# Kernel tuning notes

Measured on AMD Instinct MI355X. Metric: run time of the kernel, lower is better.

The kernel has to match this reference:

```python
import jax, jax.numpy as jnp
import numpy as np

N_NODES = 20000
N_EDGES = 160000
N_GRAPHS = 64
HIDDEN = 128
CTX = 2048
HEADS = 4
NUM_LAYERS = 3
NUM_BINS = 240
MAX_DIST = 30.0
GAMMA = 0.5
BN_EPS = 1e-5
OUT_DIM = 1024


def setup_inputs() -> dict:
    key = jax.random.key(0)
    ks = jax.random.split(key, 32)
    inp = {}
    inp["atom_types"] = jax.random.randint(ks[0], (N_NODES,), 0, 118)
    inp["pos"] = jax.random.normal(ks[1], (N_NODES, 3), dtype=jnp.float32) * 5.0
    inp["edge_index"] = jax.random.randint(ks[2], (2, N_EDGES), 0, N_NODES)
    inp["edge_attr"] = jax.random.uniform(ks[3], (N_EDGES, 5), dtype=jnp.float32)
    inp["batch"] = jnp.sort(jax.random.randint(ks[4], (N_NODES,), 0, N_GRAPHS))
    inp["context_vector"] = jax.random.normal(ks[5], (N_GRAPHS, CTX), dtype=jnp.float32)
    # initial node embedding Linear(118 -> 128)
    inp["emb_W"] = jax.random.normal(ks[6], (118, HIDDEN), dtype=jnp.float32) * 0.05
    inp["emb_b"] = jnp.zeros((HIDDEN,), jnp.float32)
    # RBF positional MLP: Linear(720->128) + BN + ReLU + Linear(128->2048)
    inp["rbf_lin1_W"] = jax.random.normal(ks[7], (3 * NUM_BINS, 128), dtype=jnp.float32) * 0.03
    inp["rbf_lin1_b"] = jnp.zeros((128,), jnp.float32)
    inp["rbf_bn_g"] = jnp.ones((128,), jnp.float32)
    inp["rbf_bn_b"] = jnp.zeros((128,), jnp.float32)
    inp["rbf_bn_m"] = jax.random.normal(ks[8], (128,), dtype=jnp.float32) * 0.1
    inp["rbf_bn_v"] = jax.random.uniform(ks[9], (128,), dtype=jnp.float32, minval=0.5, maxval=1.5)
    inp["rbf_lin2_W"] = jax.random.normal(ks[10], (128, CTX), dtype=jnp.float32) * 0.05
    inp["rbf_lin2_b"] = jnp.zeros((CTX,), jnp.float32)
    # per-layer GAT params (stacked over layers)
    in_dim = HIDDEN + CTX  # 2176
    inp["gat_W"] = jax.random.normal(ks[11], (NUM_LAYERS, in_dim, HEADS * HIDDEN), dtype=jnp.float32) * 0.02
    inp["att_src"] = jax.random.normal(ks[12], (NUM_LAYERS, HEADS, HIDDEN), dtype=jnp.float32) * 0.1
    inp["att_dst"] = jax.random.normal(ks[13], (NUM_LAYERS, HEADS, HIDDEN), dtype=jnp.float32) * 0.1
    inp["gat_bias"] = jnp.zeros((NUM_LAYERS, HIDDEN), jnp.float32)
    inp["bn_g"] = jnp.ones((NUM_LAYERS, HIDDEN), jnp.float32)
    inp["bn_b"] = jnp.zeros((NUM_LAYERS, HIDDEN), jnp.float32)
    inp["bn_m"] = jax.random.normal(ks[14], (NUM_LAYERS, HIDDEN), dtype=jnp.float32) * 0.1
    inp["bn_v"] = jax.random.uniform(ks[15], (NUM_LAYERS, HIDDEN), dtype=jnp.float32, minval=0.5, maxval=1.5)
    # final Linear(128 -> 1024)
    inp["out_W"] = jax.random.normal(ks[16], (HIDDEN, OUT_DIM), dtype=jnp.float32) * 0.05
    inp["out_b"] = jnp.zeros((OUT_DIM,), jnp.float32)
    return inp


def _bn_eval(x, g, b, m, v):
    return (x - m) * jax.lax.rsqrt(v + BN_EPS) * g + b


def _forward(atom_types, pos, edge_index, edge_attr, batch, context_vector,
             emb_W, emb_b, rbf_lin1_W, rbf_lin1_b, rbf_bn_g, rbf_bn_b, rbf_bn_m,
             rbf_bn_v, rbf_lin2_W, rbf_lin2_b, gat_W, att_src, att_dst, gat_bias,
             bn_g, bn_b, bn_m, bn_v, out_W, out_b):
    N = atom_types.shape[0]
    # initial node embedding (one-hot @ W == row gather, but keep faithful math)
    x = jax.nn.one_hot(atom_types, 118, dtype=jnp.float32) @ emb_W + emb_b  # [N,128]
    # RBF positional encoding: [N,3,num_bins] -> [N,720]
    mu = jnp.linspace(-MAX_DIST, MAX_DIST, NUM_BINS, dtype=jnp.float32)
    rbf = jnp.exp(-GAMMA * (pos[..., None] - mu) ** 2).reshape(N, 3 * NUM_BINS)
    h = jax.nn.relu(_bn_eval(rbf @ rbf_lin1_W + rbf_lin1_b, rbf_bn_g, rbf_bn_b, rbf_bn_m, rbf_bn_v))
    pos_emb = h @ rbf_lin2_W + rbf_lin2_b  # [N,2048]
    context = context_vector[batch] + pos_emb  # pos_info == 'add'
    # GAT adds self-loops by default; edge_attr is ignored (edge_dim=None)
    loops = jnp.arange(N)
    src = jnp.concatenate([edge_index[0], loops])  # message source j
    dst = jnp.concatenate([edge_index[1], loops])  # message target i
    for l in range(NUM_LAYERS):
        xc = jnp.concatenate([x, context], axis=1)                  # [N,2176]
        xs = (xc @ gat_W[l]).reshape(N, HEADS, HIDDEN)              # [N,H,C]
        a_src = jnp.einsum('nhc,hc->nh', xs, att_src[l])            # [N,H]
        a_dst = jnp.einsum('nhc,hc->nh', xs, att_dst[l])
        alpha = jax.nn.leaky_relu(a_src[src] + a_dst[dst], 0.2)     # [E+N,H]
        amax = jax.ops.segment_max(alpha, dst, num_segments=N)
        alpha = jnp.exp(alpha - amax[dst])
        denom = jax.ops.segment_sum(alpha, dst, num_segments=N)
        alpha = alpha / jnp.maximum(denom[dst], 1e-16)
        msg = xs[src] * alpha[..., None]                             # [E+N,H,C]
        agg = jax.ops.segment_sum(msg, dst, num_segments=N)          # [N,H,C]
        x_conv = agg.mean(axis=1) + gat_bias[l]                      # concat=False -> head mean
        x_conv = _bn_eval(x_conv, bn_g[l], bn_b[l], bn_m[l], bn_v[l])
        x_conv = jax.nn.gelu(x_conv, approximate=False)
        x = x + x_conv                                               # residual; dropout inactive (eval)
    out = x @ out_W + out_b                                          # [N,1024]
    return jax.ops.segment_sum(out, batch, num_segments=N_GRAPHS)    # global_add_pool -> [B,1024]


def reference(atom_types, pos, edge_index, edge_attr, batch, context_vector,
              emb_W, emb_b, rbf_lin1_W, rbf_lin1_b, rbf_bn_g, rbf_bn_b, rbf_bn_m,
              rbf_bn_v, rbf_lin2_W, rbf_lin2_b, gat_W, att_src, att_dst, gat_bias,
              bn_g, bn_b, bn_m, bn_v, out_W, out_b):
    return _forward(atom_types, pos, edge_index, edge_attr, batch, context_vector,
                    emb_W, emb_b, rbf_lin1_W, rbf_lin1_b, rbf_bn_g, rbf_bn_b,
                    rbf_bn_m, rbf_bn_v, rbf_lin2_W, rbf_lin2_b, gat_W, att_src,
                    att_dst, gat_bias, bn_g, bn_b, bn_m, bn_v, out_W, out_b)
```

## Files before the change

### kernel.cpp

```cpp
#include <hip/hip_runtime.h>
#include <hip/hip_bf16.h>
#include <cstdint>

constexpr int HIDDEN = 128, CTXD = 2048, HEADS = 4, NLAYERS = 3;
constexpr int KRBF = 720, KPAD = 736;
constexpr int KXH = 256;

typedef __bf16 bf16x8 __attribute__((ext_vector_type(8)));
typedef float f32x4 __attribute__((ext_vector_type(4)));

static __device__ __forceinline__ unsigned short f2bf(float f) {
    union { float f; unsigned u; } v; v.f = f;
    unsigned r = v.u + 0x7fffu + ((v.u >> 16) & 1u);
    return (unsigned short)(r >> 16);
}
static __device__ __forceinline__ float bf2f(unsigned short s) {
    union { unsigned u; float f; } v; v.u = ((unsigned)s) << 16; return v.f;
}

__global__ __launch_bounds__(256) void k_tr(const float* __restrict__ src,
                                            unsigned short* __restrict__ dst,
                                            int R, int C) {
    __shared__ unsigned short t[32][34];
    int b = blockIdx.z;
    int c0 = blockIdx.x * 32, r0 = blockIdx.y * 32;
    const float* s = src + (size_t)b * R * C;
    unsigned short* d = dst + (size_t)b * R * C;
    for (int rr = threadIdx.y; rr < 32; rr += 8) {
        int r = r0 + rr, c = c0 + threadIdx.x;
        unsigned short val = 0;
        if (r < R && c < C) val = f2bf(s[(size_t)r * C + c]);
        t[rr][threadIdx.x] = val;
    }
    __syncthreads();
    for (int rr = threadIdx.y; rr < 32; rr += 8) {
        int c = c0 + rr, r = r0 + threadIdx.x;
        if (c < C && r < R) d[(size_t)c * R + r] = t[threadIdx.x][rr];
    }
}

__global__ __launch_bounds__(256) void k_w2bf(const float* __restrict__ W2,
                                              unsigned short* __restrict__ W2bf) {
    int i = blockIdx.x * 256 + threadIdx.x;
    if (i < 128 * CTXD) W2bf[i] = f2bf(W2[i]);
}
__global__ __launch_bounds__(256) void k_cpre(const float* __restrict__ ctx,
                                              const float* __restrict__ b2,
                                              unsigned short* __restrict__ cpre, int NG) {
    int i = blockIdx.x * 256 + threadIdx.x;
    if (i < NG * CTXD) cpre[i] = f2bf(ctx[i] + b2[i % CTXD]);
}
__global__ __launch_bounds__(256) void k_bccopy(const unsigned short* __restrict__ gatWt,
                                                unsigned short* __restrict__ Bc) {
    int i = blockIdx.x * 256 + threadIdx.x;
    if (i >= NLAYERS * 512 * 128) return;
    int lo = i >> 7, k = i & 127;
    Bc[(size_t)lo * KXH + k] = gatWt[(size_t)lo * 2176 + k];
}

__global__ __launch_bounds__(256) void k_trW1(const float* __restrict__ W1,
                                              unsigned short* __restrict__ W1t) {
    int i = blockIdx.x * 256 + threadIdx.x;
    if (i >= 128 * KPAD) return;
    int c = i / KPAD, k = i % KPAD;
    unsigned short v = 0;
    if (k < KRBF) v = f2bf(W1[(size_t)k * 128 + c]);
    W1t[i] = v;
}

__global__ __launch_bounds__(256) void k_embed(const int* __restrict__ at,
                                               const float* __restrict__ W,
                                               const float* __restrict__ b,
                                               float* __restrict__ x,
                                               unsigned short* __restrict__ xh, int N) {
    int i = blockIdx.x * 256 + threadIdx.x;
    if (i >= N * HIDDEN) return;
    int n = i >> 7, c = i & 127;
    float v = W[(size_t)at[n] * HIDDEN + c] + b[c];
    x[i] = v;
    xh[(size_t)n * KXH + c] = f2bf(v);
}

__global__ __launch_bounds__(256) void k_rbf_mfma(const float* __restrict__ pos,
                                                  const unsigned short* __restrict__ W1t,
                                                  const float* __restrict__ b1,
                                                  const float* __restrict__ g,
                                                  const float* __restrict__ bb,
                                                  const float* __restrict__ bm,
                                                  const float* __restrict__ bv,
                                                  unsigned short* __restrict__ xh, int N) {
    constexpr int LDT = 40;
    __shared__ unsigned short As[128 * LDT];
    __shared__ unsigned short Bs[128 * LDT];
    __shared__ float ps[128 * 3];
    const int tid = threadIdx.x;
    const int lane = tid & 63, wid = tid >> 6;
    const int nb = blockIdx.x * 128;
    for (int i = tid; i < 384; i += 256) {
        int n = nb + i / 3;
        ps[i] = (n < N) ? pos[(size_t)n * 3 + (i % 3)] : 1.0e9f;
    }
    __syncthreads();
    const int sr = tid >> 1, sk = (tid & 1) * 16;
    const int wr = (wid >> 1) * 64, wc = (wid & 1) * 64;
    const int fr = lane & 15, kg = lane >> 4;
    f32x4 acc[4][4];
#pragma unroll
    for (int i = 0; i < 4; i++)
#pragma unroll
        for (int j = 0; j < 4; j++)
#pragma unroll
            for (int r = 0; r < 4; r++) acc[i][j][r] = 0.f;
    const float p0 = ps[sr * 3], p1 = ps[sr * 3 + 1], p2 = ps[sr * 3 + 2];
    const unsigned short* bp = W1t + (size_t)sr * KPAD + sk;
    uint4 bv0 = *(const uint4*)bp, bv1 = *(const uint4*)(bp + 8);
    constexpr int NST = KPAD / 32;
    for (int ks = 0; ks < NST; ++ks) {
        unsigned short av[16];
#pragma unroll
        for (int j = 0; j < 16; j++) {
            int kglob = ks * 32 + sk + j;
            float v = 0.f;
            if (kglob < KRBF) {
                int d = kglob / 240, bin = kglob % 240;
                float mu = -30.f + (60.f / 239.f) * (float)bin;
                float p = (d == 0) ? p0 : ((d == 1) ? p1 : p2);
                float df = p - mu;
                v = __expf(-0.5f * df * df);
            }
            av[j] = f2bf(v);
        }
        __syncthreads();
        *(uint4*)&As[sr * LDT + sk] = *(const uint4*)&av[0];
        *(uint4*)&As[sr * LDT + sk + 8] = *(const uint4*)&av[8];
        *(uint4*)&Bs[sr * LDT + sk] = bv0;
        *(uint4*)&Bs[sr * LDT + sk + 8] = bv1;
        __syncthreads();
        if (ks + 1 < NST) {
            const unsigned short* bp2 = W1t + (size_t)sr * KPAD + (ks + 1) * 32 + sk;
            bv0 = *(const uint4*)bp2;
            bv1 = *(const uint4*)(bp2 + 8);
        }
        bf16x8 afr[4], bfr[4];
#pragma unroll
        for (int i = 0; i < 4; i++) {
            afr[i] = *reinterpret_cast<const bf16x8*>(&As[(wr + i * 16 + fr) * LDT + kg * 8]);
            bfr[i] = *reinterpret_cast<const bf16x8*>(&Bs[(wc + i * 16 + fr) * LDT + kg * 8]);
        }
#pragma unroll
        for (int i = 0; i < 4; i++)
#pragma unroll
            for (int j = 0; j < 4; j++)
                acc[i][j] = __builtin_amdgcn_mfma_f32_16x16x32_bf16(afr[i], bfr[j], acc[i][j], 0, 0, 0);
    }
    const int rg = lane >> 4;
#pragma unroll
    for (int i = 0; i < 4; i++) {
#pragma unroll
        for (int j = 0; j < 4; j++) {
            int col = wc + j * 16 + fr;
            float sc = g[col] * rsqrtf(bv[col] + 1e-5f);
            float sh = bb[col] - bm[col] * sc;
            float bc = b1[col];
#pragma unroll
            for (int r = 0; r < 4; r++) {
                int row = nb + wr + i * 16 + rg * 4 + r;
                if (row < N) {
                    float y = (acc[i][j][r] + bc) * sc + sh;
                    y = fmaxf(y, 0.f);
                    xh[(size_t)row * KXH + 128 + col] = f2bf(y);
                }
            }
        }
    }
}

template <int MODE>
__device__ __forceinline__ void gemm_core(unsigned short* As, unsigned short* Bs,
                                          const unsigned short* __restrict__ A, int lda, int M,
                                          const unsigned short* __restrict__ Bt, int ldb, int K,
                                          void* __restrict__ Cout, int ldc,
                                          const int* __restrict__ batch,
                                          const float* __restrict__ cw,
                                          int m0, int n0) {
    constexpr int LDT = 40;
    const int tid = threadIdx.x;
    const int lane = tid & 63, wid = tid >> 6;
    const int wr = (wid >> 1) * 64, wc = (wid & 1) * 64;
    const int sr = tid >> 1, sk = (tid & 1) * 16;
    f32x4 acc[4][4];
#pragma unroll
    for (int i = 0; i < 4; i++)
#pragma unroll
        for (int j = 0; j < 4; j++)
#pragma unroll
            for (int r = 0; r < 4; r++) acc[i][j][r] = 0.f;
    const int nst = K / 32;
    const int arow = min(m0 + sr, M - 1);
    const unsigned short* ap = A + (size_t)arow * lda + sk;
    const unsigned short* bp = Bt + (size_t)(n0 + sr) * ldb + sk;
    uint4 av0 = *(const uint4*)ap, av1 = *(const uint4*)(ap + 8);
    uint4 bv0 = *(const uint4*)bp, bv1 = *(const uint4*)(bp + 8);
    const int fr = lane & 15, kg = lane >> 4;
    for (int ks = 0; ks < nst; ++ks) {
        __syncthreads();
        *(uint4*)&As[sr * LDT + sk] = av0;
        *(uint4*)&As[sr * LDT + sk + 8] = av1;
        *(uint4*)&Bs[sr * LDT + sk] = bv0;
        *(uint4*)&Bs[sr * LDT + sk + 8] = bv1;
        __syncthreads();
        if (ks + 1 < nst) {
            const unsigned short* ap2 = A + (size_t)arow * lda + (ks + 1) * 32 + sk;
            const unsigned short* bp2 = Bt + (size_t)(n0 + sr) * ldb + (ks + 1) * 32 + sk;
            av0 = *(const uint4*)ap2; av1 = *(const uint4*)(ap2 + 8);
            bv0 = *(const uint4*)bp2; bv1 = *(const uint4*)(bp2 + 8);
        }
        bf16x8 afr[4], bfr[4];
#pragma unroll
        for (int i = 0; i < 4; i++) {
            afr[i] = *reinterpret_cast<const bf16x8*>(&As[(wr + i * 16 + fr) * LDT + kg * 8]);
            bfr[i] = *reinterpret_cast<const bf16x8*>(&Bs[(wc + i * 16 + fr) * LDT + kg * 8]);
        }
#pragma unroll
        for (int i = 0; i < 4; i++)
#pragma unroll
            for (int j = 0; j < 4; j++)
                acc[i][j] = __builtin_amdgcn_mfma_f32_16x16x32_bf16(afr[i], bfr[j], acc[i][j], 0, 0, 0);
    }
    const int rg = lane >> 4;
#pragma unroll
    for (int i = 0; i < 4; i++) {
#pragma unroll
        for (int j = 0; j < 4; j++) {
            int col = n0 + wc + j * 16 + fr;
#pragma unroll
            for (int r = 0; r < 4; r++) {
                int row = m0 + wr + i * 16 + rg * 4 + r;
                if (row < M) {
                    float vv = acc[i][j][r];
                    if (MODE == 2) {
                        ((float*)Cout)[(size_t)row * ldc + col] = vv;
                    } else if (MODE == 3) {
                        vv += cw[(size_t)batch[row] * 512 + col];
                        ((unsigned short*)Cout)[(size_t)row * ldc + col] = f2bf(vv);
                    } else {
                        ((unsigned short*)Cout)[(size_t)row * ldc + col] = f2bf(vv);
                    }
                }
            }
        }
    }
}

__global__ __launch_bounds__(256) void k_gemm3(const unsigned short* __restrict__ A, int M,
                                               const unsigned short* __restrict__ Bt,
                                               unsigned short* __restrict__ C,
                                               const int* __restrict__ batch,
                                               const float* __restrict__ cw) {
    constexpr int LDT = 40;
    __shared__ unsigned short As[128 * LDT];
    __shared__ unsigned short Bs[128 * LDT];
    gemm_core<3>(As, Bs, A, KXH, M, Bt, KXH, KXH, C, 512, batch, cw,
                 blockIdx.x * 128, blockIdx.y * 128);
}

__global__ __launch_bounds__(256) void k_prep(const unsigned short* __restrict__ gatWt,
                                              const unsigned short* __restrict__ W2bf,
                                              const unsigned short* __restrict__ cpre,
                                              unsigned short* __restrict__ Bc,
                                              float* __restrict__ cW, int NG) {
    constexpr int LDT = 40;
    __shared__ unsigned short As[128 * LDT];
    __shared__ unsigned short Bs[128 * LDT];
    int z = blockIdx.z;
    if (z < 3) {
        if (blockIdx.y != 0) return;
        gemm_core<0>(As, Bs, gatWt + (size_t)z * 512 * 2176 + 128, 2176, 512,
                     W2bf, CTXD, CTXD, Bc + (size_t)z * 512 * KXH + 128, KXH,
                     nullptr, nullptr, blockIdx.x * 128, 0);
    } else {
        if (blockIdx.x != 0) return;
        int zz = z - 3;
        gemm_core<2>(As, Bs, cpre, CTXD, NG, gatWt + (size_t)zz * 512 * 2176 + 128, 2176, CTXD,
                     cW + (size_t)zz * NG * 512, 512, nullptr, nullptr, 0, blockIdx.y * 128);
    }
}

__global__ __launch_bounds__(256) void k_att(const unsigned short* __restrict__ xs,
                                             const float* __restrict__ att_s,
                                             const float* __restrict__ att_d,
                                             float* __restrict__ a_src,
                                             float* __restrict__ a_dst, int N) {
    int tid = threadIdx.x, lane = tid & 63, wid = tid >> 6;
    int n = blockIdx.x * 4 + wid;
    if (n >= N) return;
    int h = lane >> 4, c0 = (lane & 15) * 8;
    uint4 raw = *(const uint4*)(xs + (size_t)n * 512 + h * 128 + c0);
    const unsigned short* rs = (const unsigned short*)&raw;
    float ss = 0.f, sd = 0.f;
#pragma unroll
    for (int j = 0; j < 8; j++) {
        float xv = bf2f(rs[j]);
        ss += xv * att_s[h * 128 + c0 + j];
        sd += xv * att_d[h * 128 + c0 + j];
    }
#pragma unroll
    for (int d = 1; d < 16; d <<= 1) {
        ss += __shfl_xor(ss, d);
        sd += __shfl_xor(sd, d);
    }
    if ((lane & 15) == 0) {
        a_src[n * 4 + h] = ss;
        a_dst[n * 4 + h] = sd;
    }
}

__global__ void k_cnt_init(int* cnt, int N) {
    int i = blockIdx.x * 256 + threadIdx.x;
    if (i < N) cnt[i] = 1;
}
__global__ void k_cnt(const int* __restrict__ ei, int E, int* cnt) {
    int i = blockIdx.x * 256 + threadIdx.x;
    if (i < E) atomicAdd(&cnt[ei[E + i]], 1);
}
__global__ __launch_bounds__(1024) void k_scan(const int* __restrict__ cnt, int* __restrict__ rowptr,
                                               int* __restrict__ cursor, int n) {
    __shared__ int wsum[16];
    __shared__ int carry;
    int tid = threadIdx.x, lane = tid & 63, wid = tid >> 6;
    if (tid == 0) carry = 0;
    __syncthreads();
    for (int basei = 0; basei < n; basei += 1024) {
        int i = basei + tid;
        int v = (i < n) ? cnt[i] : 0;
        int s = v;
#pragma unroll
        for (int d = 1; d < 64; d <<= 1) {
            int t = __shfl_up(s, (unsigned)d);
            if (lane >= d) s += t;
        }
        if (lane == 63) wsum[wid] = s;
        __syncthreads();
        if (wid == 0 && lane < 16) {
            int ws = wsum[lane]; int t = ws;
#pragma unroll
            for (int d = 1; d < 16; d <<= 1) {
                int u = __shfl_up(t, (unsigned)d);
                if (lane >= d) t += u;
            }
            wsum[lane] = t - ws;
        }
        __syncthreads();
        int excl = carry + wsum[wid] + (s - v);
        if (i < n) { rowptr[i] = excl; cursor[i] = excl; }
        __syncthreads();
        if (tid == 1023) carry += wsum[15] + s;
        __syncthreads();
    }
    if (tid == 0) rowptr[n] = carry;
}
__global__ void k_fill(const int* __restrict__ ei, int E, int N, int* cursor, int* csrc) {
    int i = blockIdx.x * 256 + threadIdx.x;
    if (i >= E + N) return;
    int s, d;
    if (i < E) { s = ei[i]; d = ei[E + i]; }
    else { s = i - E; d = s; }
    int slot = atomicAdd(&cursor[d], 1);
    csrc[slot] = s;
}

__global__ __launch_bounds__(256) void k_agg(const int* __restrict__ rowptr,
                                             const int* __restrict__ csrc,
                                             const float* __restrict__ asrc,
                                             const float* __restrict__ adstv,
                                             const unsigned short* __restrict__ xs,
                                             const float* __restrict__ gbias,
                                             const float* __restrict__ bg,
                                             const float* __restrict__ bb,
                                             const float* __restrict__ bm,
                                             const float* __restrict__ bv,
                                             float* __restrict__ x,
                                             unsigned short* __restrict__ xh, int N) {
    __shared__ float wsh[4][64][4];
    __shared__ int ssh[4][64];
    int tid = threadIdx.x, lane = tid & 63, wid = tid >> 6;
    int n = blockIdx.x * 4 + wid;
    if (n >= N) return;
    int beg = rowptr[n], end = rowptr[n + 1];
    float4 ad = *(const float4*)(adstv + (size_t)n * 4);
    int nch = (end - beg + 63) >> 6;
    float m0 = -1e30f, m1 = -1e30f, m2 = -1e30f, m3 = -1e30f;
    float s0 = 0.f, s1 = 0.f, s2 = 0.f, s3 = 0.f;
    float a0 = -1e30f, a1 = -1e30f, a2 = -1e30f, a3 = -1e30f;
    int sv = 0;
    for (int base = beg; base < end; base += 64) {
        int idx = base + lane;
        float b0 = -1e30f, b1 = -1e30f, b2 = -1e30f, b3 = -1e30f;
        int s = 0;
        if (idx < end) {
            s = csrc[idx];
            float4 t = *(const float4*)(asrc + (size_t)s * 4);
            b0 = t.x + ad.x; b0 = b0 > 0.f ? b0 : 0.2f * b0;
            b1 = t.y + ad.y; b1 = b1 > 0.f ? b1 : 0.2f * b1;
            b2 = t.z + ad.z; b2 = b2 > 0.f ? b2 : 0.2f * b2;
            b3 = t.w + ad.w; b3 = b3 > 0.f ? b3 : 0.2f * b3;
        }
        float c0 = b0, c1 = b1, c2 = b2, c3 = b3;
#pragma unroll
        for (int d = 1; d < 64; d <<= 1) {
            c0 = fmaxf(c0, __shfl_xor(c0, d));
            c1 = fmaxf(c1, __shfl_xor(c1, d));
            c2 = fmaxf(c2, __shfl_xor(c2, d));
            c3 = fmaxf(c3, __shfl_xor(c3, d));
        }
        float nm0 = fmaxf(m0, c0), nm1 = fmaxf(m1, c1), nm2 = fmaxf(m2, c2), nm3 = fmaxf(m3, c3);
        float e0 = (idx < end) ? __expf(b0 - nm0) : 0.f;
        float e1 = (idx < end) ? __expf(b1 - nm1) : 0.f;
        float e2 = (idx < end) ? __expf(b2 - nm2) : 0.f;
        float e3 = (idx < end) ? __expf(b3 - nm3) : 0.f;
#pragma unroll
        for (int d = 1; d < 64; d <<= 1) {
            e0 += __shfl_xor(e0, d); e1 += __shfl_xor(e1, d);
            e2 += __shfl_xor(e2, d); e3 += __shfl_xor(e3, d);
        }
        s0 = s0 * __expf(m0 - nm0) + e0; m0 = nm0;
        s1 = s1 * __expf(m1 - nm1) + e1; m1 = nm1;
        s2 = s2 * __expf(m2 - nm2) + e2; m2 = nm2;
        s3 = s3 * __expf(m3 - nm3) + e3; m3 = nm3;
        a0 = b0; a1 = b1; a2 = b2; a3 = b3; sv = s;
    }
    float i0 = 1.f / fmaxf(s0, 1e-16f), i1 = 1.f / fmaxf(s1, 1e-16f);
    float i2 = 1.f / fmaxf(s2, 1e-16f), i3 = 1.f / fmaxf(s3, 1e-16f);
    const int h = lane >> 4, c0i = (lane & 15) * 8;
    float acc[8];
#pragma unroll
    for (int j = 0; j < 8; j++) acc[j] = 0.f;
    for (int base = beg; base < end; base += 64) {
        int s; float w0, w1, w2, w3;
        if (nch == 1) {
            s = sv;
            w0 = __expf(a0 - m0) * i0; w1 = __expf(a1 - m1) * i1;
            w2 = __expf(a2 - m2) * i2; w3 = __expf(a3 - m3) * i3;
        } else {
            int idx = base + lane;
            float b0 = -1e30f, b1 = -1e30f, b2 = -1e30f, b3 = -1e30f;
            s = 0;
            if (idx < end) {
                s = csrc[idx];
                float4 t = *(const float4*)(asrc + (size_t)s * 4);
                b0 = t.x + ad.x; b0 = b0 > 0.f ? b0 : 0.2f * b0;
                b1 = t.y + ad.y; b1 = b1 > 0.f ? b1 : 0.2f * b1;
                b2 = t.z + ad.z; b2 = b2 > 0.f ? b2 : 0.2f * b2;
                b3 = t.w + ad.w; b3 = b3 > 0.f ? b3 : 0.2f * b3;
            }
            w0 = __expf(b0 - m0) * i0; w1 = __expf(b1 - m1) * i1;
            w2 = __expf(b2 - m2) * i2; w3 = __expf(b3 - m3) * i3;
        }
        ssh[wid][lane] = s;
        wsh[wid][lane][0] = w0; wsh[wid][lane][1] = w1;
        wsh[wid][lane][2] = w2; wsh[wid][lane][3] = w3;
        int cnt = min(64, end - base);
        int i = 0;
        for (; i + 2 <= cnt; i += 2) {
            int sa = ssh[wid][i], sb = ssh[wid][i + 1];
            float wa = wsh[wid][i][h], wb = wsh[wid][i + 1][h];
            uint4 ra = *(const uint4*)(xs + ((size_t)sa << 9) + (h << 7) + c0i);
            uint4 rb = *(const uint4*)(xs + ((size_t)sb << 9) + (h << 7) + c0i);
            const unsigned short* qa = (const unsigned short*)&ra;
            const unsigned short* qb = (const unsigned short*)&rb;
#pragma unroll
            for (int j = 0; j < 8; j++) acc[j] += wa * bf2f(qa[j]);
#pragma unroll
            for (int j = 0; j < 8; j++) acc[j] += wb * bf2f(qb[j]);
        }
        if (i < cnt) {
            int sa = ssh[wid][i];
            float wa = wsh[wid][i][h];
            uint4 ra = *(const uint4*)(xs + ((size_t)sa << 9) + (h << 7) + c0i);
            const unsigned short* qa = (const unsigned short*)&ra;
#pragma unroll
            for (int j = 0; j < 8; j++) acc[j] += wa * bf2f(qa[j]);
        }
    }
#pragma unroll
    for (int j = 0; j < 8; j++) {
        acc[j] += __shfl_xor(acc[j], 16);
        acc[j] += __shfl_xor(acc[j], 32);
    }
    if (lane < 16) {
#pragma unroll
        for (int j = 0; j < 8; j++) {
            int c = c0i + j;
            float t = acc[j] * 0.25f + gbias[c];
            float sc = bg[c] * rsqrtf(bv[c] + 1e-5f);
            float y = (t - bm[c]) * sc + bb[c];
            float ge = 0.5f * y * (1.f + erff(y * 0.70710678118f));
            float xn = x[(size_t)n * 128 + c] + ge;
            x[(size_t)n * 128 + c] = xn;
            xh[(size_t)n * KXH + c] = f2bf(xn);
        }
    }
}

__global__ __launch_bounds__(256) void k_pool(const float* __restrict__ x,
                                              const int* __restrict__ batch,
                                              const float* __restrict__ W,
                                              const float* __restrict__ bo,
                                              float* __restrict__ out, int N) {
    __shared__ float xg[128];
    __shared__ float tmp[256];
    __shared__ int bounds[2];
    int g = blockIdx.x, tid = threadIdx.x;
    if (tid < 2) {
        int key = g + tid, lo = 0, hi = N;
        while (lo < hi) { int mid = (lo + hi) >> 1; if (batch[mid] < key) lo = mid + 1; else hi = mid; }
        bounds[tid] = lo;
    }
    __syncthreads();
    int s = bounds[0], e = bounds[1];
    int c = tid & 127, rgp = tid >> 7;
    float a = 0.f;
    for (int n = s + rgp; n < e; n += 2) a += x[(size_t)n * 128 + c];
    tmp[tid] = a;
    __syncthreads();
    if (tid < 128) xg[tid] = tmp[tid] + tmp[tid + 128];
    __syncthreads();
    float cntf = (float)(e - s);
    for (int j = tid; j < 1024; j += 256) {
        float o = cntf * bo[j];
        for (int cc = 0; cc < 128; cc++) o += xg[cc] * W[(size_t)cc * 1024 + j];
        out[(size_t)g * 1024 + j] = o;
    }
}

extern "C" void kernel_launch(void* const* d_in, const int* in_sizes, int n_in,
                              void* d_out, int out_size, void* d_ws, size_t ws_size,
                              hipStream_t stream) {
    const int N = in_sizes[0];
    const int E = in_sizes[2] / 2;
    const int NG = in_sizes[5] / CTXD;
    const int* at = (const int*)d_in[0];
    const float* pos = (const float*)d_in[1];
    const int* ei = (const int*)d_in[2];
    const int* batch = (const int*)d_in[4];
    const float* ctx = (const float*)d_in[5];
    const float* embW = (const float*)d_in[6];
    const float* embB = (const float*)d_in[7];
    const float* W1 = (const float*)d_in[8];
    const float* b1 = (const float*)d_in[9];
    const float* rg = (const float*)d_in[10];
    const float* rb = (const float*)d_in[11];
    const float* rm = (const float*)d_in[12];
    const float* rv = (const float*)d_in[13];
    const float* W2 = (const float*)d_in[14];
    const float* b2 = (const float*)d_in[15];
    const float* gatW = (const float*)d_in[16];
    const float* atts = (const float*)d_in[17];
    const float* attd = (const float*)d_in[18];
    const float* gbias = (const float*)d_in[19];
    const float* bg = (const float*)d_in[20];
    const float* bbb = (const float*)d_in[21];
    const float* bm = (const float*)d_in[22];
    const float* bv = (const float*)d_in[23];
    const float* outW = (const float*)d_in[24];
    const float* outb = (const float*)d_in[25];
    float* out = (float*)d_out;

    char* basep = (char*)d_ws;
    size_t off = 0;
    auto alloc = [&](size_t bytes) -> char* {
        char* p = basep + off;
        off = (off + bytes + 255) & ~(size_t)255;
        return p;
    };
    unsigned short* xh = (unsigned short*)alloc((size_t)N * KXH * 2);
    float* x = (float*)alloc((size_t)N * 128 * 4);
    unsigned short* xs = (unsigned short*)alloc((size_t)N * 512 * 2);
    float* a_src = (float*)alloc((size_t)N * 4 * 4);
    float* a_dst = (float*)alloc((size_t)N * 4 * 4);
    int* cnt = (int*)alloc((size_t)N * 4);
    int* rowptr = (int*)alloc((size_t)(N + 1) * 4);
    int* cursor = (int*)alloc((size_t)N * 4);
    int* csrc = (int*)alloc((size_t)(E + N) * 4);
    unsigned short* gatWt = (unsigned short*)alloc((size_t)NLAYERS * 512 * 2176 * 2);
    unsigned short* W1t = (unsigned short*)alloc((size_t)128 * KPAD * 2);
    unsigned short* W2bf = (unsigned short*)alloc((size_t)128 * CTXD * 2);
    unsigned short* cpre = (unsigned short*)alloc((size_t)NG * CTXD * 2);
    unsigned short* Bc = (unsigned short*)alloc((size_t)NLAYERS * 512 * KXH * 2);
    float* cW = (float*)alloc((size_t)NLAYERS * NG * 512 * 4);
    (void)ws_size; (void)n_in; (void)out_size;

    {
        dim3 b(32, 8);
        dim3 g1((512 + 31) / 32, (2176 + 31) / 32, NLAYERS);
        k_tr<<<g1, b, 0, stream>>>(gatW, gatWt, 2176, 512);
        k_trW1<<<(128 * KPAD + 255) / 256, 256, 0, stream>>>(W1, W1t);
        k_w2bf<<<(128 * CTXD + 255) / 256, 256, 0, stream>>>(W2, W2bf);
        k_cpre<<<(NG * CTXD + 255) / 256, 256, 0, stream>>>(ctx, b2, cpre, NG);
        k_bccopy<<<(NLAYERS * 512 * 128 + 255) / 256, 256, 0, stream>>>(gatWt, Bc);
        dim3 gp(4, 4, 6);
        k_prep<<<gp, 256, 0, stream>>>(gatWt, W2bf, cpre, Bc, cW, NG);
    }
    k_embed<<<(N * 128 + 255) / 256, 256, 0, stream>>>(at, embW, embB, x, xh, N);
    k_rbf_mfma<<<(N + 127) / 128, 256, 0, stream>>>(pos, W1t, b1, rg, rb, rm, rv, xh, N);
    k_cnt_init<<<(N + 255) / 256, 256, 0, stream>>>(cnt, N);
    k_cnt<<<(E + 255) / 256, 256, 0, stream>>>(ei, E, cnt);
    k_scan<<<1, 1024, 0, stream>>>(cnt, rowptr, cursor, N);
    k_fill<<<(E + N + 255) / 256, 256, 0, stream>>>(ei, E, N, cursor, csrc);
    {
        dim3 g((N + 127) / 128, 4, 1);
        for (int l = 0; l < NLAYERS; l++) {
            k_gemm3<<<g, 256, 0, stream>>>(xh, N, Bc + (size_t)l * 512 * KXH,
                                           xs, batch, cW + (size_t)l * NG * 512);
            k_att<<<(N + 3) / 4, 256, 0, stream>>>(xs, atts + l * HEADS * 128, attd + l * HEADS * 128,
                                                   a_src, a_dst, N);
            k_agg<<<(N + 3) / 4, 256, 0, stream>>>(rowptr, csrc, a_src, a_dst, xs,
                                                   gbias + l * 128, bg + l * 128, bbb + l * 128,
                                                   bm + l * 128, bv + l * 128, x, xh, N);
        }
    }
    k_pool<<<NG, 256, 0, stream>>>(x, batch, outW, outb, out, N);
}
```

Before: 472.1 us.

## Split GAT aggregation into edge-score, per-node softmax, and gather kernels

The fused per-node aggregation kernel is replaced by three kernels: an edge-parallel kernel that computes leaky-ReLU attention logits into a buffer, a thread-per-node softmax that normalizes them in place, and a gather kernel that reads precomputed weights and accumulates four neighbours per iteration. The aim is to drop the wave-wide shuffle reductions and shared-memory staging from the gather path and raise memory-level parallelism. In exchange it adds two launches per layer, an extra edge-sized alpha buffer plus a cdst array, and a serial per-node softmax loop that reads alpha three times.

```diff
diff --git a/kernel.cpp b/kernel.cpp
--- a/kernel.cpp
+++ b/kernel.cpp
@@ -359,7 +359,8 @@
     }
     if (tid == 0) rowptr[n] = carry;
 }
-__global__ void k_fill(const int* __restrict__ ei, int E, int N, int* cursor, int* csrc) {
+__global__ void k_fill(const int* __restrict__ ei, int E, int N, int* cursor,
+                       int* csrc, int* cdst) {
     int i = blockIdx.x * 256 + threadIdx.x;
     if (i >= E + N) return;
     int s, d;
@@ -367,120 +368,105 @@
     else { s = i - E; d = s; }
     int slot = atomicAdd(&cursor[d], 1);
     csrc[slot] = s;
-}
-
-__global__ __launch_bounds__(256) void k_agg(const int* __restrict__ rowptr,
-                                             const int* __restrict__ csrc,
-                                             const float* __restrict__ asrc,
-                                             const float* __restrict__ adstv,
-                                             const unsigned short* __restrict__ xs,
-                                             const float* __restrict__ gbias,
-                                             const float* __restrict__ bg,
-                                             const float* __restrict__ bb,
-                                             const float* __restrict__ bm,
-                                             const float* __restrict__ bv,
-                                             float* __restrict__ x,
-                                             unsigned short* __restrict__ xh, int N) {
-    __shared__ float wsh[4][64][4];
-    __shared__ int ssh[4][64];
+    cdst[slot] = d;
+}
+
+__global__ __launch_bounds__(256) void k_alpha(const int* __restrict__ csrc,
+                                               const int* __restrict__ cdst,
+                                               const float* __restrict__ a_src,
+                                               const float* __restrict__ a_dst,
+                                               float* __restrict__ alpha, int M) {
+    int i = blockIdx.x * 256 + threadIdx.x;
+    if (i >= M) return;
+    int s = csrc[i], d = cdst[i];
+    float4 as = *(const float4*)(a_src + (size_t)s * 4);
+    float4 ad = *(const float4*)(a_dst + (size_t)d * 4);
+    float4 o;
+    o.x = as.x + ad.x; o.x = o.x > 0.f ? o.x : 0.2f * o.x;
+    o.y = as.y + ad.y; o.y = o.y > 0.f ? o.y : 0.2f * o.y;
+    o.z = as.z + ad.z; o.z = o.z > 0.f ? o.z : 0.2f * o.z;
+    o.w = as.w + ad.w; o.w = o.w > 0.f ? o.w : 0.2f * o.w;
+    *(float4*)(alpha + (size_t)i * 4) = o;
+}
+
+__global__ __launch_bounds__(256) void k_soft(const int* __restrict__ rowptr,
+                                              float* __restrict__ alpha, int N) {
+    int n = blockIdx.x * 256 + threadIdx.x;
+    if (n >= N) return;
+    int beg = rowptr[n], end = rowptr[n + 1];
+    float m0 = -1e30f, m1 = -1e30f, m2 = -1e30f, m3 = -1e30f;
+    for (int e = beg; e < end; e++) {
+        float4 a = *(const float4*)(alpha + (size_t)e * 4);
+        m0 = fmaxf(m0, a.x); m1 = fmaxf(m1, a.y);
+        m2 = fmaxf(m2, a.z); m3 = fmaxf(m3, a.w);
+    }
+    float s0 = 0.f, s1 = 0.f, s2 = 0.f, s3 = 0.f;
+    for (int e = beg; e < end; e++) {
+        float4 a = *(const float4*)(alpha + (size_t)e * 4);
+        s0 += __expf(a.x - m0); s1 += __expf(a.y - m1);
+        s2 += __expf(a.z - m2); s3 += __expf(a.w - m3);
+    }
+    float i0 = 1.f / fmaxf(s0, 1e-16f), i1 = 1.f / fmaxf(s1, 1e-16f);
+    float i2 = 1.f / fmaxf(s2, 1e-16f), i3 = 1.f / fmaxf(s3, 1e-16f);
+    for (int e = beg; e < end; e++) {
+        float4 a = *(const float4*)(alpha + (size_t)e * 4);
+        float4 w;
+        w.x = __expf(a.x - m0) * i0; w.y = __expf(a.y - m1) * i1;
+        w.z = __expf(a.z - m2) * i2; w.w = __expf(a.w - m3) * i3;
+        *(float4*)(alpha + (size_t)e * 4) = w;
+    }
+}
+
+__global__ __launch_bounds__(256) void k_gather(const int* __restrict__ rowptr,
+                                                const int* __restrict__ csrc,
+                                                const float* __restrict__ alpha,
+                                                const unsigned short* __restrict__ xs,
+                                                const float* __restrict__ gbias,
+                                                const float* __restrict__ bg,
+                                                const float* __restrict__ bb,
+                                                const float* __restrict__ bm,
+                                                const float* __restrict__ bv,
+                                                float* __restrict__ x,
+                                                unsigned short* __restrict__ xh, int N) {
     int tid = threadIdx.x, lane = tid & 63, wid = tid >> 6;
     int n = blockIdx.x * 4 + wid;
     if (n >= N) return;
     int beg = rowptr[n], end = rowptr[n + 1];
-    float4 ad = *(const float4*)(adstv + (size_t)n * 4);
-    int nch = (end - beg + 63) >> 6;
-    float m0 = -1e30f, m1 = -1e30f, m2 = -1e30f, m3 = -1e30f;
-    float s0 = 0.f, s1 = 0.f, s2 = 0.f, s3 = 0.f;
-    float a0 = -1e30f, a1 = -1e30f, a2 = -1e30f, a3 = -1e30f;
-    int sv = 0;
-    for (int base = beg; base < end; base += 64) {
-        int idx = base + lane;
-        float b0 = -1e30f, b1 = -1e30f, b2 = -1e30f, b3 = -1e30f;
-        int s = 0;
-        if (idx < end) {
-            s = csrc[idx];
-            float4 t = *(const float4*)(asrc + (size_t)s * 4);
-            b0 = t.x + ad.x; b0 = b0 > 0.f ? b0 : 0.2f * b0;
-            b1 = t.y + ad.y; b1 = b1 > 0.f ? b1 : 0.2f * b1;
-            b2 = t.z + ad.z; b2 = b2 > 0.f ? b2 : 0.2f * b2;
-            b3 = t.w + ad.w; b3 = b3 > 0.f ? b3 : 0.2f * b3;
-        }
-        float c0 = b0, c1 = b1, c2 = b2, c3 = b3;
-#pragma unroll
-        for (int d = 1; d < 64; d <<= 1) {
-            c0 = fmaxf(c0, __shfl_xor(c0, d));
-            c1 = fmaxf(c1, __shfl_xor(c1, d));
-            c2 = fmaxf(c2, __shfl_xor(c2, d));
-            c3 = fmaxf(c3, __shfl_xor(c3, d));
-        }
-        float nm0 = fmaxf(m0, c0), nm1 = fmaxf(m1, c1), nm2 = fmaxf(m2, c2), nm3 = fmaxf(m3, c3);
-        float e0 = (idx < end) ? __expf(b0 - nm0) : 0.f;
-        float e1 = (idx < end) ? __expf(b1 - nm1) : 0.f;
-        float e2 = (idx < end) ? __expf(b2 - nm2) : 0.f;
-        float e3 = (idx < end) ? __expf(b3 - nm3) : 0.f;
-#pragma unroll
-        for (int d = 1; d < 64; d <<= 1) {
-            e0 += __shfl_xor(e0, d); e1 += __shfl_xor(e1, d);
-            e2 += __shfl_xor(e2, d); e3 += __shfl_xor(e3, d);
-        }
-        s0 = s0 * __expf(m0 - nm0) + e0; m0 = nm0;
-        s1 = s1 * __expf(m1 - nm1) + e1; m1 = nm1;
-        s2 = s2 * __expf(m2 - nm2) + e2; m2 = nm2;
-        s3 = s3 * __expf(m3 - nm3) + e3; m3 = nm3;
-        a0 = b0; a1 = b1; a2 = b2; a3 = b3; sv = s;
-    }
-    float i0 = 1.f / fmaxf(s0, 1e-16f), i1 = 1.f / fmaxf(s1, 1e-16f);
-    float i2 = 1.f / fmaxf(s2, 1e-16f), i3 = 1.f / fmaxf(s3, 1e-16f);
     const int h = lane >> 4, c0i = (lane & 15) * 8;
     float acc[8];
 #pragma unroll
     for (int j = 0; j < 8; j++) acc[j] = 0.f;
-    for (int base = beg; base < end; base += 64) {
-        int s; float w0, w1, w2, w3;
-        if (nch == 1) {
-            s = sv;
-            w0 = __expf(a0 - m0) * i0; w1 = __expf(a1 - m1) * i1;
-            w2 = __expf(a2 - m2) * i2; w3 = __expf(a3 - m3) * i3;
-        } else {
-            int idx = base + lane;
-            float b0 = -1e30f, b1 = -1e30f, b2 = -1e30f, b3 = -1e30f;
-            s = 0;
-            if (idx < end) {
-                s = csrc[idx];
-                float4 t = *(const float4*)(asrc + (size_t)s * 4);
-                b0 = t.x + ad.x; b0 = b0 > 0.f ? b0 : 0.2f * b0;
-                b1 = t.y + ad.y; b1 = b1 > 0.f ? b1 : 0.2f * b1;
-                b2 = t.z + ad.z; b2 = b2 > 0.f ? b2 : 0.2f * b2;
-                b3 = t.w + ad.w; b3 = b3 > 0.f ? b3 : 0.2f * b3;
-            }
-            w0 = __expf(b0 - m0) * i0; w1 = __expf(b1 - m1) * i1;
-            w2 = __expf(b2 - m2) * i2; w3 = __expf(b3 - m3) * i3;
-        }
-        ssh[wid][lane] = s;
-        wsh[wid][lane][0] = w0; wsh[wid][lane][1] = w1;
-        wsh[wid][lane][2] = w2; wsh[wid][lane][3] = w3;
-        int cnt = min(64, end - base);
-        int i = 0;
-        for (; i + 2 <= cnt; i += 2) {
-            int sa = ssh[wid][i], sb = ssh[wid][i + 1];
-            float wa = wsh[wid][i][h], wb = wsh[wid][i + 1][h];
-            uint4 ra = *(const uint4*)(xs + ((size_t)sa << 9) + (h << 7) + c0i);
-            uint4 rb = *(const uint4*)(xs + ((size_t)sb << 9) + (h << 7) + c0i);
-            const unsigned short* qa = (const unsigned short*)&ra;
-            const unsigned short* qb = (const unsigned short*)&rb;
-#pragma unroll
-            for (int j = 0; j < 8; j++) acc[j] += wa * bf2f(qa[j]);
-#pragma unroll
-            for (int j = 0; j < 8; j++) acc[j] += wb * bf2f(qb[j]);
-        }
-        if (i < cnt) {
-            int sa = ssh[wid][i];
-            float wa = wsh[wid][i][h];
-            uint4 ra = *(const uint4*)(xs + ((size_t)sa << 9) + (h << 7) + c0i);
-            const unsigned short* qa = (const unsigned short*)&ra;
-#pragma unroll
-            for (int j = 0; j < 8; j++) acc[j] += wa * bf2f(qa[j]);
-        }
+    int e = beg;
+    for (; e + 4 <= end; e += 4) {
+        int s0 = csrc[e], s1 = csrc[e + 1], s2 = csrc[e + 2], s3 = csrc[e + 3];
+        float w0 = alpha[(size_t)e * 4 + h];
+        float w1 = alpha[(size_t)(e + 1) * 4 + h];
+        float w2 = alpha[(size_t)(e + 2) * 4 + h];
+        float w3 = alpha[(size_t)(e + 3) * 4 + h];
+        uint4 r0 = *(const uint4*)(xs + ((size_t)s0 << 9) + (h << 7) + c0i);
+        uint4 r1 = *(const uint4*)(xs + ((size_t)s1 << 9) + (h << 7) + c0i);
+        uint4 r2 = *(const uint4*)(xs + ((size_t)s2 << 9) + (h << 7) + c0i);
+        uint4 r3 = *(const uint4*)(xs + ((size_t)s3 << 9) + (h << 7) + c0i);
+        const unsigned short* q0 = (const unsigned short*)&r0;
+        const unsigned short* q1 = (const unsigned short*)&r1;
+        const unsigned short* q2 = (const unsigned short*)&r2;
+        const unsigned short* q3 = (const unsigned short*)&r3;
+#pragma unroll
+        for (int j = 0; j < 8; j++) acc[j] += w0 * bf2f(q0[j]);
+#pragma unroll
+        for (int j = 0; j < 8; j++) acc[j] += w1 * bf2f(q1[j]);
+#pragma unroll
+        for (int j = 0; j < 8; j++) acc[j] += w2 * bf2f(q2[j]);
+#pragma unroll
+        for (int j = 0; j < 8; j++) acc[j] += w3 * bf2f(q3[j]);
+    }
+    for (; e < end; e++) {
+        int s0 = csrc[e];
+        float w0 = alpha[(size_t)e * 4 + h];
+        uint4 r0 = *(const uint4*)(xs + ((size_t)s0 << 9) + (h << 7) + c0i);
+        const unsigned short* q0 = (const unsigned short*)&r0;
+#pragma unroll
+        for (int j = 0; j < 8; j++) acc[j] += w0 * bf2f(q0[j]);
     }
 #pragma unroll
     for (int j = 0; j < 8; j++) {
@@ -582,6 +568,8 @@
     int* rowptr = (int*)alloc((size_t)(N + 1) * 4);
     int* cursor = (int*)alloc((size_t)N * 4);
     int* csrc = (int*)alloc((size_t)(E + N) * 4);
+    int* cdst = (int*)alloc((size_t)(E + N) * 4);
+    float* alpha = (float*)alloc((size_t)(E + N) * 4 * 4);
     unsigned short* gatWt = (unsigned short*)alloc((size_t)NLAYERS * 512 * 2176 * 2);
     unsigned short* W1t = (unsigned short*)alloc((size_t)128 * KPAD * 2);
     unsigned short* W2bf = (unsigned short*)alloc((size_t)128 * CTXD * 2);
@@ -606,17 +594,20 @@
     k_cnt_init<<<(N + 255) / 256, 256, 0, stream>>>(cnt, N);
     k_cnt<<<(E + 255) / 256, 256, 0, stream>>>(ei, E, cnt);
     k_scan<<<1, 1024, 0, stream>>>(cnt, rowptr, cursor, N);
-    k_fill<<<(E + N + 255) / 256, 256, 0, stream>>>(ei, E, N, cursor, csrc);
+    k_fill<<<(E + N + 255) / 256, 256, 0, stream>>>(ei, E, N, cursor, csrc, cdst);
     {
         dim3 g((N + 127) / 128, 4, 1);
+        const int M = E + N;
         for (int l = 0; l < NLAYERS; l++) {
             k_gemm3<<<g, 256, 0, stream>>>(xh, N, Bc + (size_t)l * 512 * KXH,
                                            xs, batch, cW + (size_t)l * NG * 512);
             k_att<<<(N + 3) / 4, 256, 0, stream>>>(xs, atts + l * HEADS * 128, attd + l * HEADS * 128,
                                                    a_src, a_dst, N);
-            k_agg<<<(N + 3) / 4, 256, 0, stream>>>(rowptr, csrc, a_src, a_dst, xs,
-                                                   gbias + l * 128, bg + l * 128, bbb + l * 128,
-                                                   bm + l * 128, bv + l * 128, x, xh, N);
+            k_alpha<<<(M + 255) / 256, 256, 0, stream>>>(csrc, cdst, a_src, a_dst, alpha, M);
+            k_soft<<<(N + 255) / 256, 256, 0, stream>>>(rowptr, alpha, N);
+            k_gather<<<(N + 3) / 4, 256, 0, stream>>>(rowptr, csrc, alpha, xs,
+                                                      gbias + l * 128, bg + l * 128, bbb + l * 128,
+                                                      bm + l * 128, bv + l * 128, x, xh, N);
         }
     }
     k_pool<<<NG, 256, 0, stream>>>(x, batch, outW, outb, out, N);
```

Result: slower. 524.4 us (+11.1%).
